# Kernel tuning notes

Hardware: AMD Instinct MI355X
Metric: run time of the kernel (lower is better)

Reference implementation:

```python
import jax, jax.numpy as jnp
import numpy as np
import math

CHANNELS = 512
N_HEADS = 8
K_CH = CHANNELS // N_HEADS            # 64 per-head dim
ROPE_D = int(K_CH * 0.5)              # 32 dims get RoPE, rest pass through
BASE = 10000


def _rope(x):
    # x: [b, h, t, dk]; rotate first ROPE_D dims (half-split style, matching the torch module)
    d = ROPE_D
    t = x.shape[2]
    theta = 1.0 / (BASE ** (jnp.arange(0, d, 2, dtype=jnp.float32) / d))      # [d/2]
    ang = jnp.arange(t, dtype=jnp.float32)[:, None] * theta[None, :]          # [t, d/2]
    ang = jnp.concatenate([ang, ang], axis=-1)                                # [t, d]
    cos = jnp.cos(ang)[None, None, :, :].astype(x.dtype)
    sin = jnp.sin(ang)[None, None, :, :].astype(x.dtype)
    x_rope, x_pass = x[..., :d], x[..., d:]
    neg_half = jnp.concatenate([-x_rope[..., d // 2:], x_rope[..., :d // 2]], axis=-1)
    return jnp.concatenate([x_rope * cos + neg_half * sin, x_pass], axis=-1)


def _split_heads(y):
    # [b, (h c), t] -> [b, h, t, c]
    b, _, t = y.shape
    return y.reshape(b, N_HEADS, K_CH, t).transpose(0, 1, 3, 2)


def setup_inputs() -> dict:
    key = jax.random.key(0)
    ks = jax.random.split(key, 10)
    B, T = 8, 1024
    w_scale = 1.0 / math.sqrt(CHANNELS)
    return {
        "x": jax.random.normal(ks[0], (B, CHANNELS, T), jnp.float32),
        "c": jax.random.normal(ks[1], (B, CHANNELS, T), jnp.float32),
        "Wq": jax.random.normal(ks[2], (CHANNELS, CHANNELS), jnp.float32) * w_scale,
        "bq": jax.random.normal(ks[3], (CHANNELS,), jnp.float32) * 0.02,
        "Wk": jax.random.normal(ks[4], (CHANNELS, CHANNELS), jnp.float32) * w_scale,
        "bk": jax.random.normal(ks[5], (CHANNELS,), jnp.float32) * 0.02,
        "Wv": jax.random.normal(ks[6], (CHANNELS, CHANNELS), jnp.float32) * w_scale,
        "bv": jax.random.normal(ks[7], (CHANNELS,), jnp.float32) * 0.02,
        "Wo": jax.random.normal(ks[8], (CHANNELS, CHANNELS), jnp.float32) * w_scale,
        "bo": jax.random.normal(ks[9], (CHANNELS,), jnp.float32) * 0.02,
    }


def reference(x, c, Wq, bq, Wk, bk, Wv, bv, Wo, bo):
    # 1x1 Conv1d == per-timestep linear over channels
    q = jnp.einsum('oc,bct->bot', Wq, x) + bq[None, :, None]
    k = jnp.einsum('oc,bct->bot', Wk, c) + bk[None, :, None]
    v = jnp.einsum('oc,bct->bot', Wv, c) + bv[None, :, None]

    q = _rope(_split_heads(q))            # [b,h,t,ck]
    k = _rope(_split_heads(k))            # [b,h,s,ck]
    v = _split_heads(v)                   # [b,h,s,ck]

    scale = 1.0 / math.sqrt(K_CH)
    scores = jnp.einsum('bhtc,bhsc->bhts', q, k) * scale
    p_attn = jax.nn.softmax(scores, axis=-1)       # dropout p=0 -> identity
    out = jnp.einsum('bhts,bhsc->bhtc', p_attn, v)

    b, _, t, _ = out.shape
    out = out.transpose(0, 1, 3, 2).reshape(b, CHANNELS, t)   # [b, (h c), t]
    return jnp.einsum('oc,bct->bot', Wo, out) + bo[None, :, None]
```

## Files before the change

### kernel.cpp

```cpp
#include <hip/hip_runtime.h>

typedef __bf16 bf16x8 __attribute__((ext_vector_type(8)));
typedef float  f32x4  __attribute__((ext_vector_type(4)));

__device__ __forceinline__ unsigned short f2bf(float f){
    union { float f; unsigned u; } v; v.f = f;
    v.u += 0x7fffu + ((v.u >> 16) & 1u);
    return (unsigned short)(v.u >> 16);
}
__device__ __forceinline__ unsigned short f2bf_trunc(float f){
    union { float f; unsigned u; } v; v.f = f;
    return (unsigned short)(v.u >> 16);
}

__global__ __launch_bounds__(256) void cvt_bf16_4(const float* __restrict__ w0, const float* __restrict__ w1,
                                                  const float* __restrict__ w2, const float* __restrict__ w3,
                                                  unsigned short* __restrict__ o0, unsigned short* __restrict__ o1,
                                                  unsigned short* __restrict__ o2, unsigned short* __restrict__ o3){
    const float* in; unsigned short* out;
    switch (blockIdx.y){
        case 0: in = w0; out = o0; break;
        case 1: in = w1; out = o1; break;
        case 2: in = w2; out = o2; break;
        default: in = w3; out = o3; break;
    }
    int i = (blockIdx.x * 256 + threadIdx.x) * 4;
    float4 v = *(const float4*)(in + i);
    ushort4 o; o.x = f2bf(v.x); o.y = f2bf(v.y); o.z = f2bf(v.z); o.w = f2bf(v.w);
    *(ushort4*)(out + i) = o;
}

__global__ __launch_bounds__(256) void transpose_cvt(const float* __restrict__ x, const float* __restrict__ c,
                                                     unsigned short* __restrict__ xt, unsigned short* __restrict__ ct){
    __shared__ float tile[64][72];
    const int z = blockIdx.z;
    const float* in = (z < 8) ? x : c;
    unsigned short* out = (z < 8) ? xt : ct;
    const int b = z & 7;
    const int t0 = blockIdx.x * 64, c0 = blockIdx.y * 64;
    const int tid = threadIdx.x;
    {
        int r = tid >> 2, q = (tid & 3) * 16;
        const float* src = in + ((size_t)b * 512 + c0 + r) * 1024 + t0 + q;
        *(float4*)&tile[r][q + 0]  = ((const float4*)src)[0];
        *(float4*)&tile[r][q + 4]  = ((const float4*)src)[1];
        *(float4*)&tile[r][q + 8]  = ((const float4*)src)[2];
        *(float4*)&tile[r][q + 12] = ((const float4*)src)[3];
    }
    __syncthreads();
    {
        int tr = tid >> 2, cj = (tid & 3) * 16;
        unsigned pw[8];
        #pragma unroll
        for (int j = 0; j < 8; j++){
            unsigned lo = f2bf(tile[cj + 2*j    ][tr]);
            unsigned hi = f2bf(tile[cj + 2*j + 1][tr]);
            pw[j] = lo | (hi << 16);
        }
        unsigned short* dst = out + ((size_t)b * 1024 + t0 + tr) * 512 + c0 + cj;
        uint4 o0 = {pw[0], pw[1], pw[2], pw[3]};
        uint4 o1 = {pw[4], pw[5], pw[6], pw[7]};
        ((uint4*)dst)[0] = o0;
        ((uint4*)dst)[1] = o1;
    }
}

template<int MODE>
__global__ __launch_bounds__(256) void gemm_bt(const unsigned short* __restrict__ A,
                                               const unsigned short* __restrict__ Bm,
                                               const float* __restrict__ bias,
                                               void* __restrict__ outp, float oscale){
    __shared__ unsigned short a_s[128][72];
    __shared__ unsigned short b_s[128][72];
    const int m0 = blockIdx.x * 128, n0 = blockIdx.y * 128;
    const int tid = threadIdx.x;
    const int wave = tid >> 6, lane = tid & 63;
    const int l15 = lane & 15, l4 = lane >> 4;
    const int mw = (wave >> 1) * 64, nw = (wave & 1) * 64;
    const f32x4 vzero = {0.f, 0.f, 0.f, 0.f};
    f32x4 acc[4][4];
    #pragma unroll
    for (int i = 0; i < 4; i++)
        #pragma unroll
        for (int j = 0; j < 4; j++) acc[i][j] = vzero;

    for (int k0 = 0; k0 < 512; k0 += 64){
        #pragma unroll
        for (int i = 0; i < 4; i++){
            int ch = i * 256 + tid;
            int row = ch >> 3, c8 = (ch & 7) * 8;
            *(uint4*)&a_s[row][c8] = *(const uint4*)(A  + (size_t)(m0 + row) * 512 + k0 + c8);
            *(uint4*)&b_s[row][c8] = *(const uint4*)(Bm + (size_t)(n0 + row) * 512 + k0 + c8);
        }
        __syncthreads();
        #pragma unroll
        for (int kk = 0; kk < 64; kk += 32){
            bf16x8 af[4], bf[4];
            #pragma unroll
            for (int mt = 0; mt < 4; mt++)
                af[mt] = *(const bf16x8*)&a_s[mw + mt*16 + l15][kk + l4*8];
            #pragma unroll
            for (int ct = 0; ct < 4; ct++)
                bf[ct] = *(const bf16x8*)&b_s[nw + ct*16 + l15][kk + l4*8];
            #pragma unroll
            for (int mt = 0; mt < 4; mt++)
                #pragma unroll
                for (int ct = 0; ct < 4; ct++)
                    acc[mt][ct] = __builtin_amdgcn_mfma_f32_16x16x32_bf16(
                        af[mt], bf[ct], acc[mt][ct], 0, 0, 0);
        }
        __syncthreads();
    }

    if (MODE == 0){
        unsigned short* out = (unsigned short*)outp;
        float bv[4];
        #pragma unroll
        for (int ct = 0; ct < 4; ct++) bv[ct] = bias[n0 + nw + ct*16 + l15];
        const float theta = __powf(10000.0f, -(float)l15 * (1.0f / 16.0f));
        #pragma unroll
        for (int mt = 0; mt < 4; mt++){
            #pragma unroll
            for (int r = 0; r < 4; r++){
                int row = m0 + mw + mt*16 + l4*4 + r;
                int t = row & 1023;
                float v[4];
                #pragma unroll
                for (int ct = 0; ct < 4; ct++) v[ct] = acc[mt][ct][r] + bv[ct];
                float sn, cn;
                __sincosf((float)t * theta, &sn, &cn);
                float r0 = v[0] * cn - v[1] * sn;
                float r1 = v[1] * cn + v[0] * sn;
                v[0] = r0; v[1] = r1;
                #pragma unroll
                for (int ct = 0; ct < 4; ct++)
                    out[(size_t)row * 512 + n0 + nw + ct*16 + l15] = f2bf(v[ct] * oscale);
            }
        }
    } else {
        #pragma unroll
        for (int mt = 0; mt < 4; mt++){
            #pragma unroll
            for (int r = 0; r < 4; r++){
                int row = m0 + mw + mt*16 + l4*4 + r;
                float bv = bias[row];
                #pragma unroll
                for (int ct = 0; ct < 4; ct++){
                    int n = n0 + nw + ct*16 + l15;
                    size_t oaddr = (size_t)(n >> 10) * 524288 + (size_t)row * 1024 + (n & 1023);
                    float val = acc[mt][ct][r] + bv;
                    if (MODE == 1) ((unsigned short*)outp)[oaddr] = f2bf(val);
                    else           ((float*)outp)[oaddr] = val;
                }
            }
        }
    }
}

__global__ __launch_bounds__(256, 3) void flash_attn(const unsigned short* __restrict__ qt,
                                                     const unsigned short* __restrict__ kt,
                                                     const unsigned short* __restrict__ vct,
                                                     unsigned short* __restrict__ attnT){
    __shared__ unsigned short k_s[2][64][72];
    __shared__ unsigned short v_s[2][64][72];
    __shared__ unsigned short p_s[4][16][72];
    const int bh = blockIdx.y, b = bh >> 3, h = bh & 7;
    const int q0 = blockIdx.x * 128;
    const int tid = threadIdx.x, wave = tid >> 6, lane = tid & 63;
    const int l15 = lane & 15, l4 = lane >> 4;
    const f32x4 vzero = {0.f, 0.f, 0.f, 0.f};

    bf16x8 qf[2][2];
    #pragma unroll
    for (int st = 0; st < 2; st++)
        #pragma unroll
        for (int kh = 0; kh < 2; kh++)
            qf[st][kh] = *(const bf16x8*)(qt + (size_t)(b*1024 + q0 + wave*32 + st*16 + l15)*512
                                             + h*64 + kh*32 + l4*8);

    f32x4 o_acc[2][4], l_acc[2];
    #pragma unroll
    for (int st = 0; st < 2; st++){
        l_acc[st] = vzero;
        #pragma unroll
        for (int dt = 0; dt < 4; dt++) o_acc[st][dt] = vzero;
    }
    const __bf16 one_bf = (__bf16)1.0f;
    const bf16x8 ones = {one_bf, one_bf, one_bf, one_bf, one_bf, one_bf, one_bf, one_bf};

    const int r0 = tid >> 3, r1 = 32 + (tid >> 3), cc = (tid & 7) * 8;
    const unsigned short* kbase = kt  + (size_t)(b*1024)*512 + h*64;
    const unsigned short* vbase = vct + (size_t)(b*512 + h*64)*1024;

    {
        uint4 ka = *(const uint4*)(kbase + (size_t)r0*512 + cc);
        uint4 kb = *(const uint4*)(kbase + (size_t)r1*512 + cc);
        uint4 va = *(const uint4*)(vbase + (size_t)r0*1024 + cc);
        uint4 vb = *(const uint4*)(vbase + (size_t)r1*1024 + cc);
        *(uint4*)&k_s[0][r0][cc] = ka; *(uint4*)&k_s[0][r1][cc] = kb;
        *(uint4*)&v_s[0][r0][cc] = va; *(uint4*)&v_s[0][r1][cc] = vb;
    }
    __syncthreads();

    for (int it = 0; it < 16; ++it){
        const int cur = it & 1, nxt = cur ^ 1;
        uint4 ka, kb, va, vb;
        if (it < 15){
            int s0n = (it + 1) * 64;
            ka = *(const uint4*)(kbase + (size_t)(s0n + r0)*512 + cc);
            kb = *(const uint4*)(kbase + (size_t)(s0n + r1)*512 + cc);
            va = *(const uint4*)(vbase + (size_t)r0*1024 + s0n + cc);
            vb = *(const uint4*)(vbase + (size_t)r1*1024 + s0n + cc);
        }
        #pragma unroll
        for (int st = 0; st < 2; st++){
            f32x4 sa[4];
            #pragma unroll
            for (int ct = 0; ct < 4; ct++) sa[ct] = vzero;
            #pragma unroll
            for (int kh = 0; kh < 2; kh++)
                #pragma unroll
                for (int ct = 0; ct < 4; ct++){
                    bf16x8 bk = *(const bf16x8*)&k_s[cur][ct*16 + l15][kh*32 + l4*8];
                    sa[ct] = __builtin_amdgcn_mfma_f32_16x16x32_bf16(qf[st][kh], bk, sa[ct], 0, 0, 0);
                }
            #pragma unroll
            for (int ct = 0; ct < 4; ct++)
                #pragma unroll
                for (int r = 0; r < 4; r++)
                    sa[ct][r] = __expf(sa[ct][r]);
            #pragma unroll
            for (int ct = 0; ct < 4; ct++)
                #pragma unroll
                for (int r = 0; r < 4; r++)
                    p_s[wave][l4*4 + r][ct*16 + l15] = f2bf_trunc(sa[ct][r]);
            bf16x8 ap0 = *(const bf16x8*)&p_s[wave][l15][l4*8];
            bf16x8 ap1 = *(const bf16x8*)&p_s[wave][l15][32 + l4*8];
            l_acc[st] = __builtin_amdgcn_mfma_f32_16x16x32_bf16(ap0, ones, l_acc[st], 0, 0, 0);
            l_acc[st] = __builtin_amdgcn_mfma_f32_16x16x32_bf16(ap1, ones, l_acc[st], 0, 0, 0);
            #pragma unroll
            for (int dt = 0; dt < 4; dt++){
                bf16x8 bv0 = *(const bf16x8*)&v_s[cur][dt*16 + l15][l4*8];
                o_acc[st][dt] = __builtin_amdgcn_mfma_f32_16x16x32_bf16(ap0, bv0, o_acc[st][dt], 0, 0, 0);
                bf16x8 bv1 = *(const bf16x8*)&v_s[cur][dt*16 + l15][32 + l4*8];
                o_acc[st][dt] = __builtin_amdgcn_mfma_f32_16x16x32_bf16(ap1, bv1, o_acc[st][dt], 0, 0, 0);
            }
        }
        if (it < 15){
            *(uint4*)&k_s[nxt][r0][cc] = ka; *(uint4*)&k_s[nxt][r1][cc] = kb;
            *(uint4*)&v_s[nxt][r0][cc] = va; *(uint4*)&v_s[nxt][r1][cc] = vb;
        }
        __syncthreads();
    }

    #pragma unroll
    for (int st = 0; st < 2; st++){
        float rl[4];
        #pragma unroll
        for (int r = 0; r < 4; r++) rl[r] = __builtin_amdgcn_rcpf(l_acc[st][r]);
        #pragma unroll
        for (int dt = 0; dt < 4; dt++)
            #pragma unroll
            for (int r = 0; r < 4; r++){
                int row = q0 + wave*32 + st*16 + l4*4 + r;
                attnT[(size_t)(b*1024 + row)*512 + h*64 + dt*16 + l15] = f2bf(o_acc[st][dt][r] * rl[r]);
            }
    }
}

extern "C" void kernel_launch(void* const* d_in, const int* in_sizes, int n_in,
                              void* d_out, int out_size, void* d_ws, size_t ws_size,
                              hipStream_t stream){
    const float* x  = (const float*)d_in[0];
    const float* c  = (const float*)d_in[1];
    const float* Wq = (const float*)d_in[2];
    const float* bq = (const float*)d_in[3];
    const float* Wk = (const float*)d_in[4];
    const float* bk = (const float*)d_in[5];
    const float* Wv = (const float*)d_in[6];
    const float* bv = (const float*)d_in[7];
    const float* Wo = (const float*)d_in[8];
    const float* bo = (const float*)d_in[9];

    unsigned short* wq_b = (unsigned short*)d_ws;
    unsigned short* wk_b = wq_b + 262144;
    unsigned short* wv_b = wk_b + 262144;
    unsigned short* wo_b = wv_b + 262144;
    unsigned short* xt   = wo_b + 262144;
    unsigned short* ct   = xt  + 4194304;
    unsigned short* qt   = ct  + 4194304;
    unsigned short* kt   = qt  + 4194304;
    unsigned short* vct  = kt  + 4194304;
    unsigned short* attnT = xt;

    cvt_bf16_4<<<dim3(256, 4), 256, 0, stream>>>(Wq, Wk, Wv, Wo, wq_b, wk_b, wv_b, wo_b);
    transpose_cvt<<<dim3(16, 8, 16), 256, 0, stream>>>(x, c, xt, ct);
    gemm_bt<0><<<dim3(64, 4), 256, 0, stream>>>(xt, wq_b, bq, qt, 0.125f);
    gemm_bt<0><<<dim3(64, 4), 256, 0, stream>>>(ct, wk_b, bk, kt, 1.0f);
    gemm_bt<1><<<dim3(4, 64), 256, 0, stream>>>(wv_b, ct, bv, vct, 1.0f);
    flash_attn<<<dim3(8, 64), 256, 0, stream>>>(qt, kt, vct, attnT);
    gemm_bt<2><<<dim3(4, 64), 256, 0, stream>>>(wo_b, attnT, bo, d_out, 1.0f);
}
```

Measured before the change: 187.7 us.

## Use direct global-to-LDS loads with XOR swizzle and merge QKV GEMMs

Replaces the register-staged global→LDS copies in the GEMMs and flash attention with global_load_lds direct transfers into an unpadded, XOR-swizzled LDS layout, so tiles no longer pass through VGPRs and bank conflicts stay low without padding. The three Q/K/V projection GEMMs are merged into one launch over a 3-wide grid, and flash attention now issues the next tile's loads asynchronously and hoists K/V fragment reads ahead of the MFMAs. Flash attention's occupancy hint drops from 3 to 2 blocks per CU, trading occupancy for more registers to hold the hoisted fragments.

```diff
diff --git a/kernel.cpp b/kernel.cpp
--- a/kernel.cpp
+++ b/kernel.cpp
@@ -11,6 +11,11 @@
 __device__ __forceinline__ unsigned short f2bf_trunc(float f){
     union { float f; unsigned u; } v; v.f = f;
     return (unsigned short)(v.u >> 16);
+}
+__device__ __forceinline__ void gl2lds16(const unsigned short* g, unsigned short* l){
+    __builtin_amdgcn_global_load_lds(
+        (const __attribute__((address_space(1))) void*)g,
+        (__attribute__((address_space(3))) void*)l, 16, 0, 0);
 }
 
 __global__ __launch_bounds__(256) void cvt_bf16_4(const float* __restrict__ w0, const float* __restrict__ w1,
@@ -65,13 +70,129 @@
     }
 }
 
-template<int MODE>
-__global__ __launch_bounds__(256) void gemm_bt(const unsigned short* __restrict__ A,
-                                               const unsigned short* __restrict__ Bm,
-                                               const float* __restrict__ bias,
-                                               void* __restrict__ outp, float oscale){
-    __shared__ unsigned short a_s[128][72];
-    __shared__ unsigned short b_s[128][72];
+__device__ __forceinline__ void gemm_mainloop(const unsigned short* __restrict__ A,
+                                              const unsigned short* __restrict__ Bm,
+                                              unsigned short* a_s, unsigned short* b_s,
+                                              int m0, int n0, int tid, f32x4 acc[4][4]){
+    const int wave = tid >> 6, lane = tid & 63;
+    const int l15 = lane & 15, l4 = lane >> 4;
+    const int mw = (wave >> 1) * 64, nw = (wave & 1) * 64;
+    const int r8 = lane >> 3, c8l = lane & 7;
+    const int csw = (c8l ^ r8) * 8;
+    const int rp = l15 & 7;
+
+    for (int k0 = 0; k0 < 512; k0 += 64){
+        #pragma unroll
+        for (int i = 0; i < 4; i++){
+            int rg = i * 4 + wave;
+            int row = rg * 8 + r8;
+            gl2lds16(A  + (size_t)(m0 + row) * 512 + k0 + csw, a_s + rg * 512);
+            gl2lds16(Bm + (size_t)(n0 + row) * 512 + k0 + csw, b_s + rg * 512);
+        }
+        __syncthreads();
+        #pragma unroll
+        for (int kk = 0; kk < 2; kk++){
+            bf16x8 af[4], bfr[4];
+            #pragma unroll
+            for (int mt = 0; mt < 4; mt++)
+                af[mt] = *(const bf16x8*)&a_s[(mw + mt*16 + l15)*64 + (((kk*4) + l4) ^ rp)*8];
+            #pragma unroll
+            for (int ct = 0; ct < 4; ct++)
+                bfr[ct] = *(const bf16x8*)&b_s[(nw + ct*16 + l15)*64 + (((kk*4) + l4) ^ rp)*8];
+            #pragma unroll
+            for (int mt = 0; mt < 4; mt++)
+                #pragma unroll
+                for (int ct = 0; ct < 4; ct++)
+                    acc[mt][ct] = __builtin_amdgcn_mfma_f32_16x16x32_bf16(
+                        af[mt], bfr[ct], acc[mt][ct], 0, 0, 0);
+        }
+        __syncthreads();
+    }
+}
+
+__global__ __launch_bounds__(256) void qkv_gemm(const unsigned short* __restrict__ xt,
+                                                const unsigned short* __restrict__ ct,
+                                                const unsigned short* __restrict__ wq,
+                                                const unsigned short* __restrict__ wk,
+                                                const unsigned short* __restrict__ wv,
+                                                const float* __restrict__ bq_,
+                                                const float* __restrict__ bk_,
+                                                const float* __restrict__ bv_,
+                                                unsigned short* __restrict__ qt,
+                                                unsigned short* __restrict__ kt,
+                                                unsigned short* __restrict__ vct){
+    __shared__ unsigned short a_s[128*64];
+    __shared__ unsigned short b_s[128*64];
+    const int z = blockIdx.y, bid = blockIdx.x;
+    const unsigned short *A, *Bm;
+    int m0, n0;
+    if (z == 0){ A = xt; Bm = wq; m0 = (bid >> 2)*128; n0 = (bid & 3)*128; }
+    else if (z == 1){ A = ct; Bm = wk; m0 = (bid >> 2)*128; n0 = (bid & 3)*128; }
+    else { A = wv; Bm = ct; m0 = (bid & 3)*128; n0 = (bid >> 2)*128; }
+    const int tid = threadIdx.x;
+    const int wave = tid >> 6, lane = tid & 63;
+    const int l15 = lane & 15, l4 = lane >> 4;
+    const int mw = (wave >> 1) * 64, nw = (wave & 1) * 64;
+    const f32x4 vzero = {0.f, 0.f, 0.f, 0.f};
+    f32x4 acc[4][4];
+    #pragma unroll
+    for (int i = 0; i < 4; i++)
+        #pragma unroll
+        for (int j = 0; j < 4; j++) acc[i][j] = vzero;
+
+    gemm_mainloop(A, Bm, a_s, b_s, m0, n0, tid, acc);
+
+    if (z < 2){
+        unsigned short* out = (z == 0) ? qt : kt;
+        const float* bias = (z == 0) ? bq_ : bk_;
+        const float oscale = (z == 0) ? 0.125f : 1.0f;
+        float bv4[4];
+        #pragma unroll
+        for (int ct2 = 0; ct2 < 4; ct2++) bv4[ct2] = bias[n0 + nw + ct2*16 + l15];
+        const float theta = __powf(10000.0f, -(float)l15 * (1.0f / 16.0f));
+        #pragma unroll
+        for (int mt = 0; mt < 4; mt++){
+            #pragma unroll
+            for (int r = 0; r < 4; r++){
+                int row = m0 + mw + mt*16 + l4*4 + r;
+                int t = row & 1023;
+                float v[4];
+                #pragma unroll
+                for (int ct2 = 0; ct2 < 4; ct2++) v[ct2] = acc[mt][ct2][r] + bv4[ct2];
+                float sn, cn;
+                __sincosf((float)t * theta, &sn, &cn);
+                float r0 = v[0] * cn - v[1] * sn;
+                float r1 = v[1] * cn + v[0] * sn;
+                v[0] = r0; v[1] = r1;
+                #pragma unroll
+                for (int ct2 = 0; ct2 < 4; ct2++)
+                    out[(size_t)row * 512 + n0 + nw + ct2*16 + l15] = f2bf(v[ct2] * oscale);
+            }
+        }
+    } else {
+        #pragma unroll
+        for (int mt = 0; mt < 4; mt++){
+            #pragma unroll
+            for (int r = 0; r < 4; r++){
+                int row = m0 + mw + mt*16 + l4*4 + r;
+                float bb = bv_[row];
+                #pragma unroll
+                for (int ct2 = 0; ct2 < 4; ct2++){
+                    int n = n0 + nw + ct2*16 + l15;
+                    size_t oaddr = (size_t)(n >> 10) * 524288 + (size_t)row * 1024 + (n & 1023);
+                    vct[oaddr] = f2bf(acc[mt][ct2][r] + bb);
+                }
+            }
+        }
+    }
+}
+
+__global__ __launch_bounds__(256) void gemm_o(const unsigned short* __restrict__ wo,
+                                              const unsigned short* __restrict__ attnT,
+                                              const float* __restrict__ bo,
+                                              float* __restrict__ out){
+    __shared__ unsigned short a_s[128*64];
+    __shared__ unsigned short b_s[128*64];
     const int m0 = blockIdx.x * 128, n0 = blockIdx.y * 128;
     const int tid = threadIdx.x;
     const int wave = tid >> 6, lane = tid & 63;
@@ -84,91 +205,42 @@
         #pragma unroll
         for (int j = 0; j < 4; j++) acc[i][j] = vzero;
 
-    for (int k0 = 0; k0 < 512; k0 += 64){
-        #pragma unroll
-        for (int i = 0; i < 4; i++){
-            int ch = i * 256 + tid;
-            int row = ch >> 3, c8 = (ch & 7) * 8;
-            *(uint4*)&a_s[row][c8] = *(const uint4*)(A  + (size_t)(m0 + row) * 512 + k0 + c8);
-            *(uint4*)&b_s[row][c8] = *(const uint4*)(Bm + (size_t)(n0 + row) * 512 + k0 + c8);
-        }
-        __syncthreads();
-        #pragma unroll
-        for (int kk = 0; kk < 64; kk += 32){
-            bf16x8 af[4], bf[4];
-            #pragma unroll
-            for (int mt = 0; mt < 4; mt++)
-                af[mt] = *(const bf16x8*)&a_s[mw + mt*16 + l15][kk + l4*8];
-            #pragma unroll
-            for (int ct = 0; ct < 4; ct++)
-                bf[ct] = *(const bf16x8*)&b_s[nw + ct*16 + l15][kk + l4*8];
-            #pragma unroll
-            for (int mt = 0; mt < 4; mt++)
-                #pragma unroll
-                for (int ct = 0; ct < 4; ct++)
-                    acc[mt][ct] = __builtin_amdgcn_mfma_f32_16x16x32_bf16(
-                        af[mt], bf[ct], acc[mt][ct], 0, 0, 0);
-        }
-        __syncthreads();
-    }
-
-    if (MODE == 0){
-        unsigned short* out = (unsigned short*)outp;
-        float bv[4];
-        #pragma unroll
-        for (int ct = 0; ct < 4; ct++) bv[ct] = bias[n0 + nw + ct*16 + l15];
-        const float theta = __powf(10000.0f, -(float)l15 * (1.0f / 16.0f));
-        #pragma unroll
-        for (int mt = 0; mt < 4; mt++){
-            #pragma unroll
-            for (int r = 0; r < 4; r++){
-                int row = m0 + mw + mt*16 + l4*4 + r;
-                int t = row & 1023;
-                float v[4];
-                #pragma unroll
-                for (int ct = 0; ct < 4; ct++) v[ct] = acc[mt][ct][r] + bv[ct];
-                float sn, cn;
-                __sincosf((float)t * theta, &sn, &cn);
-                float r0 = v[0] * cn - v[1] * sn;
-                float r1 = v[1] * cn + v[0] * sn;
-                v[0] = r0; v[1] = r1;
-                #pragma unroll
-                for (int ct = 0; ct < 4; ct++)
-                    out[(size_t)row * 512 + n0 + nw + ct*16 + l15] = f2bf(v[ct] * oscale);
-            }
-        }
-    } else {
-        #pragma unroll
-        for (int mt = 0; mt < 4; mt++){
-            #pragma unroll
-            for (int r = 0; r < 4; r++){
-                int row = m0 + mw + mt*16 + l4*4 + r;
-                float bv = bias[row];
-                #pragma unroll
-                for (int ct = 0; ct < 4; ct++){
-                    int n = n0 + nw + ct*16 + l15;
-                    size_t oaddr = (size_t)(n >> 10) * 524288 + (size_t)row * 1024 + (n & 1023);
-                    float val = acc[mt][ct][r] + bv;
-                    if (MODE == 1) ((unsigned short*)outp)[oaddr] = f2bf(val);
-                    else           ((float*)outp)[oaddr] = val;
-                }
-            }
-        }
-    }
-}
-
-__global__ __launch_bounds__(256, 3) void flash_attn(const unsigned short* __restrict__ qt,
+    gemm_mainloop(wo, attnT, a_s, b_s, m0, n0, tid, acc);
+
+    #pragma unroll
+    for (int mt = 0; mt < 4; mt++){
+        #pragma unroll
+        for (int r = 0; r < 4; r++){
+            int row = m0 + mw + mt*16 + l4*4 + r;
+            float bb = bo[row];
+            #pragma unroll
+            for (int ct2 = 0; ct2 < 4; ct2++){
+                int n = n0 + nw + ct2*16 + l15;
+                size_t oaddr = (size_t)(n >> 10) * 524288 + (size_t)row * 1024 + (n & 1023);
+                out[oaddr] = acc[mt][ct2][r] + bb;
+            }
+        }
+    }
+}
+
+__global__ __launch_bounds__(256, 2) void flash_attn(const unsigned short* __restrict__ qt,
                                                      const unsigned short* __restrict__ kt,
                                                      const unsigned short* __restrict__ vct,
                                                      unsigned short* __restrict__ attnT){
-    __shared__ unsigned short k_s[2][64][72];
-    __shared__ unsigned short v_s[2][64][72];
+    __shared__ unsigned short k_s[2][64*64];
+    __shared__ unsigned short v_s[2][64*64];
     __shared__ unsigned short p_s[4][16][72];
     const int bh = blockIdx.y, b = bh >> 3, h = bh & 7;
     const int q0 = blockIdx.x * 128;
     const int tid = threadIdx.x, wave = tid >> 6, lane = tid & 63;
     const int l15 = lane & 15, l4 = lane >> 4;
+    const int r8 = lane >> 3, c8l = lane & 7;
+    const int csw = (c8l ^ r8) * 8;
+    const int rp = l15 & 7;
     const f32x4 vzero = {0.f, 0.f, 0.f, 0.f};
+
+    const unsigned short* kbase = kt  + (size_t)(b*1024)*512 + h*64;
+    const unsigned short* vbase = vct + (size_t)(b*512 + h*64)*1024;
 
     bf16x8 qf[2][2];
     #pragma unroll
@@ -188,30 +260,36 @@
     const __bf16 one_bf = (__bf16)1.0f;
     const bf16x8 ones = {one_bf, one_bf, one_bf, one_bf, one_bf, one_bf, one_bf, one_bf};
 
-    const int r0 = tid >> 3, r1 = 32 + (tid >> 3), cc = (tid & 7) * 8;
-    const unsigned short* kbase = kt  + (size_t)(b*1024)*512 + h*64;
-    const unsigned short* vbase = vct + (size_t)(b*512 + h*64)*1024;
-
-    {
-        uint4 ka = *(const uint4*)(kbase + (size_t)r0*512 + cc);
-        uint4 kb = *(const uint4*)(kbase + (size_t)r1*512 + cc);
-        uint4 va = *(const uint4*)(vbase + (size_t)r0*1024 + cc);
-        uint4 vb = *(const uint4*)(vbase + (size_t)r1*1024 + cc);
-        *(uint4*)&k_s[0][r0][cc] = ka; *(uint4*)&k_s[0][r1][cc] = kb;
-        *(uint4*)&v_s[0][r0][cc] = va; *(uint4*)&v_s[0][r1][cc] = vb;
-    }
+    auto stage = [&](int tile, int buf){
+        const int s0n = tile * 64;
+        #pragma unroll
+        for (int i = 0; i < 2; i++){
+            int rg = i * 4 + wave;
+            int row = rg * 8 + r8;
+            gl2lds16(kbase + (size_t)(s0n + row)*512 + csw, &k_s[buf][rg*512]);
+            gl2lds16(vbase + (size_t)row*1024 + s0n + csw, &v_s[buf][rg*512]);
+        }
+    };
+
+    stage(0, 0);
     __syncthreads();
 
     for (int it = 0; it < 16; ++it){
-        const int cur = it & 1, nxt = cur ^ 1;
-        uint4 ka, kb, va, vb;
-        if (it < 15){
-            int s0n = (it + 1) * 64;
-            ka = *(const uint4*)(kbase + (size_t)(s0n + r0)*512 + cc);
-            kb = *(const uint4*)(kbase + (size_t)(s0n + r1)*512 + cc);
-            va = *(const uint4*)(vbase + (size_t)r0*1024 + s0n + cc);
-            vb = *(const uint4*)(vbase + (size_t)r1*1024 + s0n + cc);
-        }
+        const int cur = it & 1;
+        if (it < 15) stage(it + 1, cur ^ 1);
+
+        bf16x8 kf[2][4], vf[2][4];
+        #pragma unroll
+        for (int kh = 0; kh < 2; kh++)
+            #pragma unroll
+            for (int ct = 0; ct < 4; ct++)
+                kf[kh][ct] = *(const bf16x8*)&k_s[cur][(ct*16 + l15)*64 + ((kh*4 + l4) ^ rp)*8];
+        #pragma unroll
+        for (int sh = 0; sh < 2; sh++)
+            #pragma unroll
+            for (int dt = 0; dt < 4; dt++)
+                vf[sh][dt] = *(const bf16x8*)&v_s[cur][(dt*16 + l15)*64 + ((sh*4 + l4) ^ rp)*8];
+
         #pragma unroll
         for (int st = 0; st < 2; st++){
             f32x4 sa[4];
@@ -220,10 +298,8 @@
             #pragma unroll
             for (int kh = 0; kh < 2; kh++)
                 #pragma unroll
-                for (int ct = 0; ct < 4; ct++){
-                    bf16x8 bk = *(const bf16x8*)&k_s[cur][ct*16 + l15][kh*32 + l4*8];
-                    sa[ct] = __builtin_amdgcn_mfma_f32_16x16x32_bf16(qf[st][kh], bk, sa[ct], 0, 0, 0);
-                }
+                for (int ct = 0; ct < 4; ct++)
+                    sa[ct] = __builtin_amdgcn_mfma_f32_16x16x32_bf16(qf[st][kh], kf[kh][ct], sa[ct], 0, 0, 0);
             #pragma unroll
             for (int ct = 0; ct < 4; ct++)
                 #pragma unroll
@@ -240,15 +316,9 @@
             l_acc[st] = __builtin_amdgcn_mfma_f32_16x16x32_bf16(ap1, ones, l_acc[st], 0, 0, 0);
             #pragma unroll
             for (int dt = 0; dt < 4; dt++){
-                bf16x8 bv0 = *(const bf16x8*)&v_s[cur][dt*16 + l15][l4*8];
-                o_acc[st][dt] = __builtin_amdgcn_mfma_f32_16x16x32_bf16(ap0, bv0, o_acc[st][dt], 0, 0, 0);
-                bf16x8 bv1 = *(const bf16x8*)&v_s[cur][dt*16 + l15][32 + l4*8];
-                o_acc[st][dt] = __builtin_amdgcn_mfma_f32_16x16x32_bf16(ap1, bv1, o_acc[st][dt], 0, 0, 0);
-            }
-        }
-        if (it < 15){
-            *(uint4*)&k_s[nxt][r0][cc] = ka; *(uint4*)&k_s[nxt][r1][cc] = kb;
-            *(uint4*)&v_s[nxt][r0][cc] = va; *(uint4*)&v_s[nxt][r1][cc] = vb;
+                o_acc[st][dt] = __builtin_amdgcn_mfma_f32_16x16x32_bf16(ap0, vf[0][dt], o_acc[st][dt], 0, 0, 0);
+                o_acc[st][dt] = __builtin_amdgcn_mfma_f32_16x16x32_bf16(ap1, vf[1][dt], o_acc[st][dt], 0, 0, 0);
+            }
         }
         __syncthreads();
     }
@@ -295,9 +365,7 @@
 
     cvt_bf16_4<<<dim3(256, 4), 256, 0, stream>>>(Wq, Wk, Wv, Wo, wq_b, wk_b, wv_b, wo_b);
     transpose_cvt<<<dim3(16, 8, 16), 256, 0, stream>>>(x, c, xt, ct);
-    gemm_bt<0><<<dim3(64, 4), 256, 0, stream>>>(xt, wq_b, bq, qt, 0.125f);
-    gemm_bt<0><<<dim3(64, 4), 256, 0, stream>>>(ct, wk_b, bk, kt, 1.0f);
-    gemm_bt<1><<<dim3(4, 64), 256, 0, stream>>>(wv_b, ct, bv, vct, 1.0f);
+    qkv_gemm<<<dim3(256, 3), 256, 0, stream>>>(xt, ct, wq_b, wk_b, wv_b, bq, bk, bv, qt, kt, vct);
     flash_attn<<<dim3(8, 64), 256, 0, stream>>>(qt, kt, vct, attnT);
-    gemm_bt<2><<<dim3(4, 64), 256, 0, stream>>>(wo_b, attnT, bo, d_out, 1.0f);
-}
+    gemm_o<<<dim3(4, 64), 256, 0, stream>>>(wo_b, attnT, bo, (float*)d_out);
+}
```

Result: faster. 172.9 us (-7.9%).
